# Kernel tuning notes

Measured on AMD Instinct MI355X. Metric: run time of the kernel, lower is better.

Reference implementation:

```python
import jax, jax.numpy as jnp
import numpy as np
import math

B, T, C, H = 2, 2048, 1024, 16
D = C // H
EPS = 1e-5

def _layer_norm(x, w, b):
    m = jnp.mean(x, axis=-1, keepdims=True)
    v = jnp.mean((x - m) ** 2, axis=-1, keepdims=True)
    return (x - m) * jax.lax.rsqrt(v + EPS) * w + b

def setup_inputs() -> dict:
    key = jax.random.key(0)
    ks = jax.random.split(key, 8)
    s_attn = 1.0 / math.sqrt(C)
    s_fc = 1.0 / math.sqrt(C)
    s_fc2 = 1.0 / math.sqrt(4 * C)
    return {
        "x": jax.random.normal(ks[0], (B, T, C), dtype=jnp.float32),
        "ln1_w": jnp.ones((C,), jnp.float32),
        "ln1_b": jnp.zeros((C,), jnp.float32),
        "w_qkv": jax.random.normal(ks[1], (C, 3 * C), jnp.float32) * s_attn,  # [in,out]
        "b_qkv": jnp.zeros((3 * C,), jnp.float32),
        "w_proj": jax.random.normal(ks[2], (C, C), jnp.float32) * s_attn,
        "b_proj": jnp.zeros((C,), jnp.float32),
        "ln2_w": jnp.ones((C,), jnp.float32),
        "ln2_b": jnp.zeros((C,), jnp.float32),
        "w_fc": jax.random.normal(ks[3], (C, 4 * C), jnp.float32) * s_fc,
        "b_fc": jnp.zeros((4 * C,), jnp.float32),
        "w_fc2": jax.random.normal(ks[4], (4 * C, C), jnp.float32) * s_fc2,
        "b_fc2": jnp.zeros((C,), jnp.float32),
    }

def reference(x, ln1_w, ln1_b, w_qkv, b_qkv, w_proj, b_proj,
              ln2_w, ln2_b, w_fc, b_fc, w_fc2, b_fc2):
    # --- attention branch ---
    h = _layer_norm(x, ln1_w, ln1_b)
    qkv = h @ w_qkv + b_qkv                      # [B,T,3C]
    q, k, v = jnp.split(qkv, 3, axis=-1)
    # [B,T,C] -> [B,H,T,D]
    q = q.reshape(B, T, H, D).transpose(0, 2, 1, 3)
    k = k.reshape(B, T, H, D).transpose(0, 2, 1, 3)
    v = v.reshape(B, T, H, D).transpose(0, 2, 1, 3)
    scale = 1.0 / math.sqrt(D)
    scores = jnp.einsum("bhtd,bhsd->bhts", q, k) * scale  # [B,H,T,T]
    causal = jnp.tril(jnp.ones((T, T), dtype=bool))
    scores = jnp.where(causal, scores, -jnp.inf)
    attn_w = jax.nn.softmax(scores, axis=-1)     # dropout_p = 0.0
    attn_out = jnp.einsum("bhts,bhsd->bhtd", attn_w, v)
    attn_out = attn_out.transpose(0, 2, 1, 3).reshape(B, T, C)
    attn_out = attn_out @ w_proj + b_proj
    x = x + attn_out
    # --- MLP branch ---
    h2 = _layer_norm(x, ln2_w, ln2_b)
    h2 = jax.nn.gelu(h2 @ w_fc + b_fc, approximate=False)
    x = x + (h2 @ w_fc2 + b_fc2)
    return x, jnp.mean(attn_w, axis=0)           # ([B,T,C], [H,T,T])
```

## Files before the change

### kernel.cpp

```cpp
#include <hip/hip_runtime.h>
#include <cmath>

#define BB 2
#define TT 2048
#define CC 1024
#define HH 16
#define DD 64

typedef unsigned short u16;
typedef __attribute__((ext_vector_type(8))) short bf16x8;
typedef __attribute__((ext_vector_type(4))) float f32x4;

__device__ __forceinline__ u16 f2bf(float f) {
    union { float f; unsigned u; } v; v.f = f;
    return (u16)((v.u + 0x7fff + ((v.u >> 16) & 1)) >> 16);
}

__device__ __forceinline__ float bf2f(u16 h) {
    union { unsigned u; float f; } v; v.u = ((unsigned)h) << 16;
    return v.f;
}

__device__ __forceinline__ float gelu_exact(float v) {
    return 0.5f * v * (1.0f + erff(v * 0.70710678118654752440f));
}

__device__ __forceinline__ void glds16(const void* g, void* l) {
    __builtin_amdgcn_global_load_lds(
        (const __attribute__((address_space(1))) void*)g,
        (__attribute__((address_space(3))) void*)l, 16, 0, 0);
}

__global__ __launch_bounds__(256) void wcvt_kernel(const float* __restrict__ W,
                                                   u16* __restrict__ WT,
                                                   int K, int N) {
    __shared__ u16 t[64][65];
    const int n0 = blockIdx.x * 64, k0 = blockIdx.y * 64;
    const int tid = threadIdx.x;
    const int c = tid & 63;
#pragma unroll
    for (int it = 0; it < 16; ++it) {
        int r = it * 4 + (tid >> 6);
        t[c][r] = f2bf(W[(size_t)(k0 + r) * N + n0 + c]);
    }
    __syncthreads();
#pragma unroll
    for (int it = 0; it < 16; ++it) {
        int r = it * 4 + (tid >> 6);
        WT[(size_t)(n0 + r) * K + k0 + c] = t[r][c];
    }
}

__global__ __launch_bounds__(256) void ln_kernel(const float* __restrict__ x,
                                                 const float* __restrict__ w,
                                                 const float* __restrict__ b,
                                                 u16* __restrict__ out) {
    const int row = blockIdx.x;
    const int tid = threadIdx.x;
    const float* xr = x + (size_t)row * CC;
    u16* orow = out + (size_t)row * CC;

    __shared__ float red[256];

    float v[4];
#pragma unroll
    for (int i = 0; i < 4; ++i) v[i] = xr[tid + i * 256];

    red[tid] = v[0] + v[1] + v[2] + v[3];
    __syncthreads();
    for (int off = 128; off > 0; off >>= 1) {
        if (tid < off) red[tid] += red[tid + off];
        __syncthreads();
    }
    const float mean = red[0] * (1.0f / CC);
    __syncthreads();

    float d[4], sq = 0.f;
#pragma unroll
    for (int i = 0; i < 4; ++i) { d[i] = v[i] - mean; sq += d[i] * d[i]; }
    red[tid] = sq;
    __syncthreads();
    for (int off = 128; off > 0; off >>= 1) {
        if (tid < off) red[tid] += red[tid + off];
        __syncthreads();
    }
    const float rstd = rsqrtf(red[0] * (1.0f / CC) + 1e-5f);

#pragma unroll
    for (int i = 0; i < 4; ++i) {
        int c = tid + i * 256;
        orow[c] = f2bf(d[i] * rstd * w[c] + b[c]);
    }
}

template <int EPI, int OUTBF, int WM, int WN, int FI, int FJ>
__global__ __launch_bounds__(256) void gemm_mfma(const u16* __restrict__ A,
                                                 const u16* __restrict__ BT,
                                                 const float* __restrict__ bias,
                                                 const float* __restrict__ res,
                                                 void* __restrict__ out,
                                                 int M, int N, int K) {
    constexpr int TM = WM * FI * 16;
    constexpr int TN = WN * FJ * 16;
    __shared__ u16 As[TM * 32];
    __shared__ u16 Bs[TN * 32];

    const int tid = threadIdx.x;
    const int lane = tid & 63;
    const int w = tid >> 6;
    const int wr = w / WN, wc = w % WN;
    const int m16 = lane & 15;
    const int quad = lane >> 4;

    const int bm = blockIdx.y * TM;
    const int bn = blockIdx.x * TN;

    f32x4 acc[FI][FJ] = {};

    for (int k0 = 0; k0 < K; k0 += 32) {
#pragma unroll
        for (int it = 0; it < TM / 64; ++it) {
            int cb = w * (TM / 64) * 64 + it * 64;
            int q = cb + lane;
            glds16(&A[(size_t)(bm + (q >> 2)) * K + k0 + (q & 3) * 8], &As[cb * 8]);
        }
#pragma unroll
        for (int it = 0; it < TN / 64; ++it) {
            int cb = w * (TN / 64) * 64 + it * 64;
            int q = cb + lane;
            glds16(&BT[(size_t)(bn + (q >> 2)) * K + k0 + (q & 3) * 8], &Bs[cb * 8]);
        }
        __syncthreads();

        bf16x8 a[FI], b[FJ];
#pragma unroll
        for (int i = 0; i < FI; ++i)
            a[i] = *(const bf16x8*)&As[(wr * FI * 16 + 16 * i + m16) * 32 + quad * 8];
#pragma unroll
        for (int j = 0; j < FJ; ++j)
            b[j] = *(const bf16x8*)&Bs[(wc * FJ * 16 + 16 * j + m16) * 32 + quad * 8];
#pragma unroll
        for (int i = 0; i < FI; ++i)
#pragma unroll
            for (int j = 0; j < FJ; ++j)
                acc[i][j] = __builtin_amdgcn_mfma_f32_16x16x32_bf16(a[i], b[j], acc[i][j], 0, 0, 0);
        __syncthreads();
    }

#pragma unroll
    for (int i = 0; i < FI; ++i) {
        const int row = bm + wr * FI * 16 + 16 * i + quad * 4;
#pragma unroll
        for (int j = 0; j < FJ; ++j) {
            const int col = bn + wc * FJ * 16 + 16 * j + m16;
            const float bv = bias[col];
#pragma unroll
            for (int r = 0; r < 4; ++r) {
                float v = acc[i][j][r] + bv;
                if (EPI == 1) v = gelu_exact(v);
                if (EPI == 2) v += res[(size_t)(row + r) * N + col];
                if (OUTBF) ((u16*)out)[(size_t)(row + r) * N + col] = f2bf(v);
                else ((float*)out)[(size_t)(row + r) * N + col] = v;
            }
        }
    }
}

__global__ __launch_bounds__(256) void qkvcvt_kernel(const float* __restrict__ qkv,
                                                     u16* __restrict__ Khg,
                                                     u16* __restrict__ Klg,
                                                     u16* __restrict__ VTg) {
    const int idx = blockIdx.x;
    const int st = idx & 31;
    const int h = (idx >> 5) & 15;
    const int b = idx >> 9;
    const int tid = threadIdx.x;
    const size_t TC3 = 3 * CC;

    const float* kbase = qkv + (size_t)b * TT * TC3 + (size_t)st * 64 * TC3 + CC + h * DD;
    const float* vbase = kbase + CC;
    u16* kh = Khg + (size_t)idx * 4096;
    u16* kl = Klg + (size_t)idx * 4096;
    u16* vt = VTg + (size_t)idx * 4096;

    __shared__ u16 lvt[64][65];

#pragma unroll
    for (int it = 0; it < 4; ++it) {
        int e = tid + it * 256;
        int s = e >> 4, c4 = e & 15;
        float4 v = *reinterpret_cast<const float4*>(kbase + (size_t)s * TC3 + c4 * 4);
        float fv[4] = {v.x, v.y, v.z, v.w};
        u16 hh[4], ll[4];
#pragma unroll
        for (int i = 0; i < 4; ++i) {
            union { float f; unsigned u; } tb; tb.f = fv[i];
            hh[i] = (u16)(tb.u >> 16);
            ll[i] = f2bf(fv[i] - bf2f(hh[i]));
        }
        int col = (c4 * 4) ^ ((s & 7) << 3);
        *reinterpret_cast<ushort4*>(&kh[s * 64 + col]) = make_ushort4(hh[0], hh[1], hh[2], hh[3]);
        *reinterpret_cast<ushort4*>(&kl[s * 64 + col]) = make_ushort4(ll[0], ll[1], ll[2], ll[3]);
        float4 vv = *reinterpret_cast<const float4*>(vbase + (size_t)s * TC3 + c4 * 4);
        lvt[c4 * 4 + 0][s] = f2bf(vv.x);
        lvt[c4 * 4 + 1][s] = f2bf(vv.y);
        lvt[c4 * 4 + 2][s] = f2bf(vv.z);
        lvt[c4 * 4 + 3][s] = f2bf(vv.w);
    }
    __syncthreads();
#pragma unroll
    for (int it = 0; it < 4; ++it) {
        int e = tid + it * 256;
        int d = e >> 4, s4 = (e & 15) * 4;
        ushort4 o = make_ushort4(lvt[d][s4], lvt[d][s4 + 1], lvt[d][s4 + 2], lvt[d][s4 + 3]);
        *reinterpret_cast<ushort4*>(&vt[d * 64 + (s4 ^ ((d & 7) << 3))]) = o;
    }
}

__global__ __launch_bounds__(256) void attn_kernel(const float* __restrict__ qkv,
                                                   const u16* __restrict__ Khg,
                                                   const u16* __restrict__ Klg,
                                                   const u16* __restrict__ VTg,
                                                   float* __restrict__ attn_mean,
                                                   u16* __restrict__ attn_out) {
    const int lid = blockIdx.x;
    const int u = lid & 255;
    const int h = u & 15;
    const int ta = u >> 4;
    const int tt = (lid < 256) ? ta : 31 - ta;
    const int t0 = tt * 64;

    const int tid = threadIdx.x;
    const int lane = tid & 63;
    const int w = tid >> 6;
    const int m16 = lane & 15;
    const int quad = lane >> 4;
    const size_t TC3 = 3 * CC;

    __shared__ u16 Ks[2][2][64][64];
    __shared__ u16 VTs[2][64][64];

    const int arow = w * 16 + m16;
    const int sw = (m16 & 7) << 3;
    const int rbase = w * 16 + quad * 4;

    auto toff = [&](int b, int st) -> size_t {
        return ((size_t)((b * 16 + h) * 32 + st)) * 4096;
    };

    auto stage_tile = [&](const u16* g, u16* l) {
        glds16(g + w * 1024 + lane * 8, l + w * 1024);
        glds16(g + w * 1024 + 512 + lane * 8, l + w * 1024 + 512);
    };

    bf16x8 qh[2][2], ql[2][2];
#pragma unroll
    for (int b = 0; b < 2; ++b) {
        const float* qp = qkv + (size_t)b * TT * TC3 + (size_t)(t0 + arow) * TC3 + h * DD;
#pragma unroll
        for (int ks = 0; ks < 2; ++ks) {
            float4 v0 = *reinterpret_cast<const float4*>(qp + ks * 32 + quad * 8);
            float4 v1 = *reinterpret_cast<const float4*>(qp + ks * 32 + quad * 8 + 4);
            float f[8] = {v0.x, v0.y, v0.z, v0.w, v1.x, v1.y, v1.z, v1.w};
            union { bf16x8 v; u16 s[8]; } H, L;
#pragma unroll
            for (int i = 0; i < 8; ++i) {
                float fv = f[i] * 0.125f;
                union { float f; unsigned u; } tb; tb.f = fv;
                u16 hh = (u16)(tb.u >> 16);
                H.s[i] = hh;
                L.s[i] = f2bf(fv - bf2f(hh));
            }
            qh[b][ks] = H.v;
            ql[b][ks] = L.v;
        }
    }

    auto compute_S = [&](const bf16x8 (&QH)[2], const bf16x8 (&QL)[2],
                         const u16 (*KH)[64], const u16 (*KL)[64],
                         f32x4 (&acc)[4], bool diag) {
#pragma unroll
        for (int ks = 0; ks < 2; ++ks) {
#pragma unroll
            for (int j = 0; j < 4; ++j) {
                const int co = (ks * 32 + quad * 8) ^ sw;
                bf16x8 bh = *(const bf16x8*)&KH[j * 16 + m16][co];
                bf16x8 bl = *(const bf16x8*)&KL[j * 16 + m16][co];
                acc[j] = __builtin_amdgcn_mfma_f32_16x16x32_bf16(QH[ks], bh, acc[j], 0, 0, 0);
                acc[j] = __builtin_amdgcn_mfma_f32_16x16x32_bf16(QL[ks], bh, acc[j], 0, 0, 0);
                acc[j] = __builtin_amdgcn_mfma_f32_16x16x32_bf16(QH[ks], bl, acc[j], 0, 0, 0);
            }
        }
        if (diag) {
#pragma unroll
            for (int j = 0; j < 4; ++j)
#pragma unroll
                for (int r = 0; r < 4; ++r)
                    if (j * 16 + m16 > rbase + r) acc[j][r] = -INFINITY;
        }
    };

    auto pv_acc = [&](f32x4 (&O)[4], const u16 (*Ps)[64], const u16 (*VT)[64]) {
#pragma unroll
        for (int ks = 0; ks < 2; ++ks) {
            const int co = (ks * 32 + quad * 8) ^ sw;
            bf16x8 a = *(const bf16x8*)&Ps[arow][co];
#pragma unroll
            for (int j = 0; j < 4; ++j) {
                bf16x8 bv = *(const bf16x8*)&VT[j * 16 + m16][co];
                O[j] = __builtin_amdgcn_mfma_f32_16x16x32_bf16(a, bv, O[j], 0, 0, 0);
            }
        }
    };

    float m_r[2][4], l_r[2][4];
#pragma unroll
    for (int b = 0; b < 2; ++b)
#pragma unroll
        for (int r = 0; r < 4; ++r) { m_r[b][r] = -INFINITY; l_r[b][r] = 0.f; }

    for (int st = 0; st <= tt; ++st) {
        __syncthreads();
        stage_tile(Khg + toff(0, st), &Ks[0][0][0][0]);
        stage_tile(Klg + toff(0, st), &Ks[0][1][0][0]);
        stage_tile(Khg + toff(1, st), &Ks[1][0][0][0]);
        stage_tile(Klg + toff(1, st), &Ks[1][1][0][0]);
        __syncthreads();
        const bool diag = (st == tt);
#pragma unroll
        for (int b = 0; b < 2; ++b) {
            f32x4 acc[4] = {};
            compute_S(qh[b], ql[b], Ks[b][0], Ks[b][1], acc, diag);
#pragma unroll
            for (int r = 0; r < 4; ++r) {
                float t = fmaxf(fmaxf(acc[0][r], acc[1][r]), fmaxf(acc[2][r], acc[3][r]));
                t = fmaxf(t, __shfl_xor(t, 1));
                t = fmaxf(t, __shfl_xor(t, 2));
                t = fmaxf(t, __shfl_xor(t, 4));
                t = fmaxf(t, __shfl_xor(t, 8));
                const float mn = fmaxf(m_r[b][r], t);
                float s = __expf(acc[0][r] - mn) + __expf(acc[1][r] - mn) +
                          __expf(acc[2][r] - mn) + __expf(acc[3][r] - mn);
                s += __shfl_xor(s, 1);
                s += __shfl_xor(s, 2);
                s += __shfl_xor(s, 4);
                s += __shfl_xor(s, 8);
                l_r[b][r] = l_r[b][r] * __expf(m_r[b][r] - mn) + s;
                m_r[b][r] = mn;
            }
        }
    }
#pragma unroll
    for (int b = 0; b < 2; ++b)
#pragma unroll
        for (int r = 0; r < 4; ++r) l_r[b][r] = 1.0f / l_r[b][r];

    f32x4 O0[4] = {}, O1[4] = {};
    for (int st = 0; st <= tt; ++st) {
        const int s0 = st * 64;
        const bool diag = (st == tt);
        __syncthreads();
        stage_tile(Khg + toff(0, st), &Ks[0][0][0][0]);
        stage_tile(Klg + toff(0, st), &Ks[0][1][0][0]);
        stage_tile(Khg + toff(1, st), &Ks[1][0][0][0]);
        stage_tile(Klg + toff(1, st), &Ks[1][1][0][0]);
        stage_tile(VTg + toff(0, st), &VTs[0][0][0]);
        stage_tile(VTg + toff(1, st), &VTs[1][0][0]);
        __syncthreads();

        f32x4 a0[4] = {}, a1[4] = {};
        compute_S(qh[0], ql[0], Ks[0][0], Ks[0][1], a0, diag);
        compute_S(qh[1], ql[1], Ks[1][0], Ks[1][1], a1, diag);

#pragma unroll
        for (int j = 0; j < 4; ++j)
#pragma unroll
            for (int r = 0; r < 4; ++r) {
                a0[j][r] = __expf(a0[j][r] - m_r[0][r]) * l_r[0][r];
                a1[j][r] = __expf(a1[j][r] - m_r[1][r]) * l_r[1][r];
            }

#pragma unroll
        for (int r = 0; r < 4; ++r) {
            float* mrow = attn_mean + ((size_t)h * TT + t0 + rbase + r) * TT + s0;
#pragma unroll
            for (int j = 0; j < 4; ++j)
                mrow[j * 16 + m16] = 0.5f * (a0[j][r] + a1[j][r]);
        }

        __syncthreads();

#pragma unroll
        for (int r = 0; r < 4; ++r) {
            const int prow = rbase + r;
            const int psw = (prow & 7) << 3;
#pragma unroll
            for (int j = 0; j < 4; ++j) {
                Ks[0][0][prow][(j * 16 + m16) ^ psw] = f2bf(a0[j][r]);
                Ks[1][0][prow][(j * 16 + m16) ^ psw] = f2bf(a1[j][r]);
            }
        }
        pv_acc(O0, Ks[0][0], VTs[0]);
        pv_acc(O1, Ks[1][0], VTs[1]);
    }

#pragma unroll
    for (int r = 0; r < 4; ++r) {
        const int trow = t0 + rbase + r;
#pragma unroll
        for (int j = 0; j < 4; ++j) {
            attn_out[((size_t)0 * TT + trow) * CC + h * DD + j * 16 + m16] = f2bf(O0[j][r]);
            attn_out[((size_t)1 * TT + trow) * CC + h * DD + j * 16 + m16] = f2bf(O1[j][r]);
        }
    }

    const int c0 = (tt + 1) * 64;
    const float4 z4 = make_float4(0.f, 0.f, 0.f, 0.f);
    for (int r = 0; r < 64; ++r) {
        float* row = attn_mean + ((size_t)h * TT + t0 + r) * TT;
        for (int c = c0 + tid * 4; c < TT; c += 1024)
            *reinterpret_cast<float4*>(row + c) = z4;
    }
}

extern "C" void kernel_launch(void* const* d_in, const int* in_sizes, int n_in,
                              void* d_out, int out_size, void* d_ws, size_t ws_size,
                              hipStream_t stream) {
    const float* x      = (const float*)d_in[0];
    const float* ln1_w  = (const float*)d_in[1];
    const float* ln1_b  = (const float*)d_in[2];
    const float* w_qkv  = (const float*)d_in[3];
    const float* b_qkv  = (const float*)d_in[4];
    const float* w_proj = (const float*)d_in[5];
    const float* b_proj = (const float*)d_in[6];
    const float* ln2_w  = (const float*)d_in[7];
    const float* ln2_b  = (const float*)d_in[8];
    const float* w_fc   = (const float*)d_in[9];
    const float* b_fc   = (const float*)d_in[10];
    const float* w_fc2  = (const float*)d_in[11];
    const float* b_fc2  = (const float*)d_in[12];

    float* out_x    = (float*)d_out;
    float* out_attn = out_x + (size_t)BB * TT * CC;

    char* wp = (char*)d_ws;
    u16* wT_qkv = (u16*)wp;  wp += (size_t)3072 * 1024 * 2;
    u16* wT_proj = (u16*)wp; wp += (size_t)1024 * 1024 * 2;
    u16* wT_fc  = (u16*)wp;  wp += (size_t)4096 * 1024 * 2;
    u16* wT_fc2 = (u16*)wp;  wp += (size_t)1024 * 4096 * 2;
    u16* h_ln   = (u16*)wp;  wp += (size_t)4096 * 1024 * 2;
    u16* att_o  = (u16*)wp;  wp += (size_t)4096 * 1024 * 2;
    u16* h2     = (u16*)wp;  wp += (size_t)4096 * 4096 * 2;
    float* qkv  = (float*)wp; wp += (size_t)4096 * 3072 * 4;
    float* x1   = (float*)wp; wp += (size_t)4096 * 1024 * 4;

    u16* Khg = h2;
    u16* Klg = Khg + (size_t)1024 * 4096;
    u16* VTg = Klg + (size_t)1024 * 4096;

    const int M = BB * TT;

    wcvt_kernel<<<dim3(3072 / 64, 1024 / 64), 256, 0, stream>>>(w_qkv, wT_qkv, 1024, 3072);
    wcvt_kernel<<<dim3(1024 / 64, 1024 / 64), 256, 0, stream>>>(w_proj, wT_proj, 1024, 1024);
    wcvt_kernel<<<dim3(4096 / 64, 1024 / 64), 256, 0, stream>>>(w_fc, wT_fc, 1024, 4096);
    wcvt_kernel<<<dim3(1024 / 64, 4096 / 64), 256, 0, stream>>>(w_fc2, wT_fc2, 4096, 1024);

    ln_kernel<<<M, 256, 0, stream>>>(x, ln1_w, ln1_b, h_ln);
    gemm_mfma<0, 0, 2, 2, 4, 4><<<dim3(3072 / 128, M / 128), 256, 0, stream>>>(
        h_ln, wT_qkv, b_qkv, nullptr, qkv, M, 3072, 1024);
    qkvcvt_kernel<<<1024, 256, 0, stream>>>(qkv, Khg, Klg, VTg);
    attn_kernel<<<512, 256, 0, stream>>>(qkv, Khg, Klg, VTg, out_attn, att_o);
    gemm_mfma<2, 0, 4, 1, 2, 4><<<dim3(1024 / 64, M / 128), 256, 0, stream>>>(
        att_o, wT_proj, b_proj, x, x1, M, 1024, 1024);
    ln_kernel<<<M, 256, 0, stream>>>(x1, ln2_w, ln2_b, h_ln);
    gemm_mfma<1, 1, 2, 2, 4, 4><<<dim3(4096 / 128, M / 128), 256, 0, stream>>>(
        h_ln, wT_fc, b_fc, nullptr, h2, M, 4096, 1024);
    gemm_mfma<2, 0, 4, 1, 2, 4><<<dim3(1024 / 64, M / 128), 256, 0, stream>>>(
        h2, wT_fc2, b_fc2, x1, out_x, M, 1024, 4096);
}
```

Before: 719.0 us.

## Switch attention to fp16 single-pass MFMA, double-buffer K/V, warp-level layernorm

Attention QK^T previously used a split-bf16 hi/lo scheme with three MFMAs per product. It now converts Q, K and V to fp16 and issues one f16 MFMA per product, which removes the low-part K buffer and two thirds of the score MFMAs. K and V tiles are double-buffered so the next tile's global-to-LDS load overlaps compute. LayerNorm now does one row per wavefront with float4 loads and shuffle reductions, and the proj and fc2 GEMMs use 128x128 tiles. fp16 trades the hi/lo accuracy for narrower range, which could affect the attention-weight tolerance.

```diff
diff --git a/kernel.cpp b/kernel.cpp
--- a/kernel.cpp
+++ b/kernel.cpp
@@ -9,6 +9,7 @@
 
 typedef unsigned short u16;
 typedef __attribute__((ext_vector_type(8))) short bf16x8;
+typedef __attribute__((ext_vector_type(8))) _Float16 f16x8;
 typedef __attribute__((ext_vector_type(4))) float f32x4;
 
 __device__ __forceinline__ u16 f2bf(float f) {
@@ -16,9 +17,9 @@
     return (u16)((v.u + 0x7fff + ((v.u >> 16) & 1)) >> 16);
 }
 
-__device__ __forceinline__ float bf2f(u16 h) {
-    union { unsigned u; float f; } v; v.u = ((unsigned)h) << 16;
-    return v.f;
+__device__ __forceinline__ u16 f2h(float f) {
+    union { _Float16 h; u16 u; } v; v.h = (_Float16)f;
+    return v.u;
 }
 
 __device__ __forceinline__ float gelu_exact(float v) {
@@ -55,41 +56,44 @@
                                                  const float* __restrict__ w,
                                                  const float* __restrict__ b,
                                                  u16* __restrict__ out) {
-    const int row = blockIdx.x;
     const int tid = threadIdx.x;
+    const int lane = tid & 63;
+    const int row = blockIdx.x * 4 + (tid >> 6);
     const float* xr = x + (size_t)row * CC;
     u16* orow = out + (size_t)row * CC;
 
-    __shared__ float red[256];
-
-    float v[4];
-#pragma unroll
-    for (int i = 0; i < 4; ++i) v[i] = xr[tid + i * 256];
-
-    red[tid] = v[0] + v[1] + v[2] + v[3];
-    __syncthreads();
-    for (int off = 128; off > 0; off >>= 1) {
-        if (tid < off) red[tid] += red[tid + off];
-        __syncthreads();
-    }
-    const float mean = red[0] * (1.0f / CC);
-    __syncthreads();
-
-    float d[4], sq = 0.f;
-#pragma unroll
-    for (int i = 0; i < 4; ++i) { d[i] = v[i] - mean; sq += d[i] * d[i]; }
-    red[tid] = sq;
-    __syncthreads();
-    for (int off = 128; off > 0; off >>= 1) {
-        if (tid < off) red[tid] += red[tid + off];
-        __syncthreads();
-    }
-    const float rstd = rsqrtf(red[0] * (1.0f / CC) + 1e-5f);
-
-#pragma unroll
-    for (int i = 0; i < 4; ++i) {
-        int c = tid + i * 256;
-        orow[c] = f2bf(d[i] * rstd * w[c] + b[c]);
+    float4 v[4];
+#pragma unroll
+    for (int k = 0; k < 4; ++k)
+        v[k] = *reinterpret_cast<const float4*>(xr + k * 256 + lane * 4);
+
+    float s = 0.f;
+#pragma unroll
+    for (int k = 0; k < 4; ++k) s += v[k].x + v[k].y + v[k].z + v[k].w;
+#pragma unroll
+    for (int off = 1; off < 64; off <<= 1) s += __shfl_xor(s, off);
+    const float mean = s * (1.0f / CC);
+
+    float sq = 0.f;
+#pragma unroll
+    for (int k = 0; k < 4; ++k) {
+        float dx = v[k].x - mean, dy = v[k].y - mean, dz = v[k].z - mean, dw = v[k].w - mean;
+        sq += dx * dx + dy * dy + dz * dz + dw * dw;
+    }
+#pragma unroll
+    for (int off = 1; off < 64; off <<= 1) sq += __shfl_xor(sq, off);
+    const float rstd = rsqrtf(sq * (1.0f / CC) + 1e-5f);
+
+#pragma unroll
+    for (int k = 0; k < 4; ++k) {
+        const int c = k * 256 + lane * 4;
+        float4 w4 = *reinterpret_cast<const float4*>(w + c);
+        float4 b4 = *reinterpret_cast<const float4*>(b + c);
+        ushort4 o = make_ushort4(f2bf((v[k].x - mean) * rstd * w4.x + b4.x),
+                                 f2bf((v[k].y - mean) * rstd * w4.y + b4.y),
+                                 f2bf((v[k].z - mean) * rstd * w4.z + b4.z),
+                                 f2bf((v[k].w - mean) * rstd * w4.w + b4.w));
+        *reinterpret_cast<ushort4*>(orow + c) = o;
     }
 }
 
@@ -167,8 +171,7 @@
 }
 
 __global__ __launch_bounds__(256) void qkvcvt_kernel(const float* __restrict__ qkv,
-                                                     u16* __restrict__ Khg,
-                                                     u16* __restrict__ Klg,
+                                                     u16* __restrict__ Kg,
                                                      u16* __restrict__ VTg) {
     const int idx = blockIdx.x;
     const int st = idx & 31;
@@ -179,8 +182,7 @@
 
     const float* kbase = qkv + (size_t)b * TT * TC3 + (size_t)st * 64 * TC3 + CC + h * DD;
     const float* vbase = kbase + CC;
-    u16* kh = Khg + (size_t)idx * 4096;
-    u16* kl = Klg + (size_t)idx * 4096;
+    u16* kg = Kg + (size_t)idx * 4096;
     u16* vt = VTg + (size_t)idx * 4096;
 
     __shared__ u16 lvt[64][65];
@@ -190,22 +192,14 @@
         int e = tid + it * 256;
         int s = e >> 4, c4 = e & 15;
         float4 v = *reinterpret_cast<const float4*>(kbase + (size_t)s * TC3 + c4 * 4);
-        float fv[4] = {v.x, v.y, v.z, v.w};
-        u16 hh[4], ll[4];
-#pragma unroll
-        for (int i = 0; i < 4; ++i) {
-            union { float f; unsigned u; } tb; tb.f = fv[i];
-            hh[i] = (u16)(tb.u >> 16);
-            ll[i] = f2bf(fv[i] - bf2f(hh[i]));
-        }
         int col = (c4 * 4) ^ ((s & 7) << 3);
-        *reinterpret_cast<ushort4*>(&kh[s * 64 + col]) = make_ushort4(hh[0], hh[1], hh[2], hh[3]);
-        *reinterpret_cast<ushort4*>(&kl[s * 64 + col]) = make_ushort4(ll[0], ll[1], ll[2], ll[3]);
+        *reinterpret_cast<ushort4*>(&kg[s * 64 + col]) =
+            make_ushort4(f2h(v.x), f2h(v.y), f2h(v.z), f2h(v.w));
         float4 vv = *reinterpret_cast<const float4*>(vbase + (size_t)s * TC3 + c4 * 4);
-        lvt[c4 * 4 + 0][s] = f2bf(vv.x);
-        lvt[c4 * 4 + 1][s] = f2bf(vv.y);
-        lvt[c4 * 4 + 2][s] = f2bf(vv.z);
-        lvt[c4 * 4 + 3][s] = f2bf(vv.w);
+        lvt[c4 * 4 + 0][s] = f2h(vv.x);
+        lvt[c4 * 4 + 1][s] = f2h(vv.y);
+        lvt[c4 * 4 + 2][s] = f2h(vv.z);
+        lvt[c4 * 4 + 3][s] = f2h(vv.w);
     }
     __syncthreads();
 #pragma unroll
@@ -218,8 +212,7 @@
 }
 
 __global__ __launch_bounds__(256) void attn_kernel(const float* __restrict__ qkv,
-                                                   const u16* __restrict__ Khg,
-                                                   const u16* __restrict__ Klg,
+                                                   const u16* __restrict__ Kg,
                                                    const u16* __restrict__ VTg,
                                                    float* __restrict__ attn_mean,
                                                    u16* __restrict__ attn_out) {
@@ -237,8 +230,7 @@
     const int quad = lane >> 4;
     const size_t TC3 = 3 * CC;
 
-    __shared__ u16 Ks[2][2][64][64];
-    __shared__ u16 VTs[2][64][64];
+    __shared__ u16 smem[2][4][4096];
 
     const int arow = w * 16 + m16;
     const int sw = (m16 & 7) << 3;
@@ -247,13 +239,24 @@
     auto toff = [&](int b, int st) -> size_t {
         return ((size_t)((b * 16 + h) * 32 + st)) * 4096;
     };
+    auto KSL = [&](int buf, int b) -> u16 (*)[64] { return (u16(*)[64]) & smem[buf][b][0]; };
+    auto VSL = [&](int buf, int b) -> u16 (*)[64] { return (u16(*)[64]) & smem[buf][2 + b][0]; };
 
     auto stage_tile = [&](const u16* g, u16* l) {
         glds16(g + w * 1024 + lane * 8, l + w * 1024);
         glds16(g + w * 1024 + 512 + lane * 8, l + w * 1024 + 512);
     };
-
-    bf16x8 qh[2][2], ql[2][2];
+    auto stage_K2 = [&](int buf, int st) {
+        stage_tile(Kg + toff(0, st), &smem[buf][0][0]);
+        stage_tile(Kg + toff(1, st), &smem[buf][1][0]);
+    };
+    auto stage_KV4 = [&](int buf, int st) {
+        stage_K2(buf, st);
+        stage_tile(VTg + toff(0, st), &smem[buf][2][0]);
+        stage_tile(VTg + toff(1, st), &smem[buf][3][0]);
+    };
+
+    f16x8 qh[2][2];
 #pragma unroll
     for (int b = 0; b < 2; ++b) {
         const float* qp = qkv + (size_t)b * TT * TC3 + (size_t)(t0 + arow) * TC3 + h * DD;
@@ -262,33 +265,22 @@
             float4 v0 = *reinterpret_cast<const float4*>(qp + ks * 32 + quad * 8);
             float4 v1 = *reinterpret_cast<const float4*>(qp + ks * 32 + quad * 8 + 4);
             float f[8] = {v0.x, v0.y, v0.z, v0.w, v1.x, v1.y, v1.z, v1.w};
-            union { bf16x8 v; u16 s[8]; } H, L;
-#pragma unroll
-            for (int i = 0; i < 8; ++i) {
-                float fv = f[i] * 0.125f;
-                union { float f; unsigned u; } tb; tb.f = fv;
-                u16 hh = (u16)(tb.u >> 16);
-                H.s[i] = hh;
-                L.s[i] = f2bf(fv - bf2f(hh));
-            }
+            union { f16x8 v; u16 s[8]; } H;
+#pragma unroll
+            for (int i = 0; i < 8; ++i) H.s[i] = f2h(f[i] * 0.125f);
             qh[b][ks] = H.v;
-            ql[b][ks] = L.v;
-        }
-    }
-
-    auto compute_S = [&](const bf16x8 (&QH)[2], const bf16x8 (&QL)[2],
-                         const u16 (*KH)[64], const u16 (*KL)[64],
+        }
+    }
+
+    auto compute_S = [&](const f16x8 (&QH)[2], const u16 (*KT)[64],
                          f32x4 (&acc)[4], bool diag) {
 #pragma unroll
         for (int ks = 0; ks < 2; ++ks) {
+            const int co = (ks * 32 + quad * 8) ^ sw;
 #pragma unroll
             for (int j = 0; j < 4; ++j) {
-                const int co = (ks * 32 + quad * 8) ^ sw;
-                bf16x8 bh = *(const bf16x8*)&KH[j * 16 + m16][co];
-                bf16x8 bl = *(const bf16x8*)&KL[j * 16 + m16][co];
-                acc[j] = __builtin_amdgcn_mfma_f32_16x16x32_bf16(QH[ks], bh, acc[j], 0, 0, 0);
-                acc[j] = __builtin_amdgcn_mfma_f32_16x16x32_bf16(QL[ks], bh, acc[j], 0, 0, 0);
-                acc[j] = __builtin_amdgcn_mfma_f32_16x16x32_bf16(QH[ks], bl, acc[j], 0, 0, 0);
+                f16x8 bh = *(const f16x8*)&KT[j * 16 + m16][co];
+                acc[j] = __builtin_amdgcn_mfma_f32_16x16x32_f16(QH[ks], bh, acc[j], 0, 0, 0);
             }
         }
         if (diag) {
@@ -304,11 +296,11 @@
 #pragma unroll
         for (int ks = 0; ks < 2; ++ks) {
             const int co = (ks * 32 + quad * 8) ^ sw;
-            bf16x8 a = *(const bf16x8*)&Ps[arow][co];
+            f16x8 a = *(const f16x8*)&Ps[arow][co];
 #pragma unroll
             for (int j = 0; j < 4; ++j) {
-                bf16x8 bv = *(const bf16x8*)&VT[j * 16 + m16][co];
-                O[j] = __builtin_amdgcn_mfma_f32_16x16x32_bf16(a, bv, O[j], 0, 0, 0);
+                f16x8 bv = *(const f16x8*)&VT[j * 16 + m16][co];
+                O[j] = __builtin_amdgcn_mfma_f32_16x16x32_f16(a, bv, O[j], 0, 0, 0);
             }
         }
     };
@@ -319,18 +311,16 @@
 #pragma unroll
         for (int r = 0; r < 4; ++r) { m_r[b][r] = -INFINITY; l_r[b][r] = 0.f; }
 
+    stage_K2(0, 0);
     for (int st = 0; st <= tt; ++st) {
+        const int cur = st & 1;
         __syncthreads();
-        stage_tile(Khg + toff(0, st), &Ks[0][0][0][0]);
-        stage_tile(Klg + toff(0, st), &Ks[0][1][0][0]);
-        stage_tile(Khg + toff(1, st), &Ks[1][0][0][0]);
-        stage_tile(Klg + toff(1, st), &Ks[1][1][0][0]);
-        __syncthreads();
+        if (st + 1 <= tt) stage_K2(cur ^ 1, st + 1);
         const bool diag = (st == tt);
 #pragma unroll
         for (int b = 0; b < 2; ++b) {
             f32x4 acc[4] = {};
-            compute_S(qh[b], ql[b], Ks[b][0], Ks[b][1], acc, diag);
+            compute_S(qh[b], KSL(cur, b), acc, diag);
 #pragma unroll
             for (int r = 0; r < 4; ++r) {
                 float t = fmaxf(fmaxf(acc[0][r], acc[1][r]), fmaxf(acc[2][r], acc[3][r]));
@@ -350,27 +340,24 @@
             }
         }
     }
+    __syncthreads();
 #pragma unroll
     for (int b = 0; b < 2; ++b)
 #pragma unroll
         for (int r = 0; r < 4; ++r) l_r[b][r] = 1.0f / l_r[b][r];
 
     f32x4 O0[4] = {}, O1[4] = {};
+    stage_KV4(0, 0);
     for (int st = 0; st <= tt; ++st) {
+        const int cur = st & 1;
         const int s0 = st * 64;
         const bool diag = (st == tt);
         __syncthreads();
-        stage_tile(Khg + toff(0, st), &Ks[0][0][0][0]);
-        stage_tile(Klg + toff(0, st), &Ks[0][1][0][0]);
-        stage_tile(Khg + toff(1, st), &Ks[1][0][0][0]);
-        stage_tile(Klg + toff(1, st), &Ks[1][1][0][0]);
-        stage_tile(VTg + toff(0, st), &VTs[0][0][0]);
-        stage_tile(VTg + toff(1, st), &VTs[1][0][0]);
-        __syncthreads();
+        if (st + 1 <= tt) stage_KV4(cur ^ 1, st + 1);
 
         f32x4 a0[4] = {}, a1[4] = {};
-        compute_S(qh[0], ql[0], Ks[0][0], Ks[0][1], a0, diag);
-        compute_S(qh[1], ql[1], Ks[1][0], Ks[1][1], a1, diag);
+        compute_S(qh[0], KSL(cur, 0), a0, diag);
+        compute_S(qh[1], KSL(cur, 1), a1, diag);
 
 #pragma unroll
         for (int j = 0; j < 4; ++j)
@@ -390,18 +377,20 @@
 
         __syncthreads();
 
+        u16(*P0s)[64] = KSL(cur, 0);
+        u16(*P1s)[64] = KSL(cur, 1);
 #pragma unroll
         for (int r = 0; r < 4; ++r) {
             const int prow = rbase + r;
             const int psw = (prow & 7) << 3;
 #pragma unroll
             for (int j = 0; j < 4; ++j) {
-                Ks[0][0][prow][(j * 16 + m16) ^ psw] = f2bf(a0[j][r]);
-                Ks[1][0][prow][(j * 16 + m16) ^ psw] = f2bf(a1[j][r]);
-            }
-        }
-        pv_acc(O0, Ks[0][0], VTs[0]);
-        pv_acc(O1, Ks[1][0], VTs[1]);
+                P0s[prow][(j * 16 + m16) ^ psw] = f2h(a0[j][r]);
+                P1s[prow][(j * 16 + m16) ^ psw] = f2h(a1[j][r]);
+            }
+        }
+        pv_acc(O0, P0s, VSL(cur, 0));
+        pv_acc(O1, P1s, VSL(cur, 1));
     }
 
 #pragma unroll
@@ -454,9 +443,8 @@
     float* qkv  = (float*)wp; wp += (size_t)4096 * 3072 * 4;
     float* x1   = (float*)wp; wp += (size_t)4096 * 1024 * 4;
 
-    u16* Khg = h2;
-    u16* Klg = Khg + (size_t)1024 * 4096;
-    u16* VTg = Klg + (size_t)1024 * 4096;
+    u16* Kg  = h2;
+    u16* VTg = Kg + (size_t)1024 * 4096;
 
     const int M = BB * TT;
 
@@ -465,16 +453,16 @@
     wcvt_kernel<<<dim3(4096 / 64, 1024 / 64), 256, 0, stream>>>(w_fc, wT_fc, 1024, 4096);
     wcvt_kernel<<<dim3(1024 / 64, 4096 / 64), 256, 0, stream>>>(w_fc2, wT_fc2, 4096, 1024);
 
-    ln_kernel<<<M, 256, 0, stream>>>(x, ln1_w, ln1_b, h_ln);
+    ln_kernel<<<M / 4, 256, 0, stream>>>(x, ln1_w, ln1_b, h_ln);
     gemm_mfma<0, 0, 2, 2, 4, 4><<<dim3(3072 / 128, M / 128), 256, 0, stream>>>(
         h_ln, wT_qkv, b_qkv, nullptr, qkv, M, 3072, 1024);
-    qkvcvt_kernel<<<1024, 256, 0, stream>>>(qkv, Khg, Klg, VTg);
-    attn_kernel<<<512, 256, 0, stream>>>(qkv, Khg, Klg, VTg, out_attn, att_o);
-    gemm_mfma<2, 0, 4, 1, 2, 4><<<dim3(1024 / 64, M / 128), 256, 0, stream>>>(
+    qkvcvt_kernel<<<1024, 256, 0, stream>>>(qkv, Kg, VTg);
+    attn_kernel<<<512, 256, 0, stream>>>(qkv, Kg, VTg, out_attn, att_o);
+    gemm_mfma<2, 0, 2, 2, 4, 4><<<dim3(1024 / 128, M / 128), 256, 0, stream>>>(
         att_o, wT_proj, b_proj, x, x1, M, 1024, 1024);
-    ln_kernel<<<M, 256, 0, stream>>>(x1, ln2_w, ln2_b, h_ln);
+    ln_kernel<<<M / 4, 256, 0, stream>>>(x1, ln2_w, ln2_b, h_ln);
     gemm_mfma<1, 1, 2, 2, 4, 4><<<dim3(4096 / 128, M / 128), 256, 0, stream>>>(
         h_ln, wT_fc, b_fc, nullptr, h2, M, 4096, 1024);
-    gemm_mfma<2, 0, 4, 1, 2, 4><<<dim3(1024 / 64, M / 128), 256, 0, stream>>>(
+    gemm_mfma<2, 0, 2, 2, 4, 4><<<dim3(1024 / 128, M / 128), 256, 0, stream>>>(
         h2, wT_fc2, b_fc2, x1, out_x, M, 1024, 4096);
 }
```

Measured after the change: 729.8 us. No clear change (+1.5%).
